# Kernel tuning notes

Measured on AMD Instinct MI355X. Metric: run time of the kernel, lower is better.

The kernel has to match this reference:

```python
import jax, jax.numpy as jnp
import numpy as np
import math

NUM_HEADS = 16
NUM_KV_HEADS = 4
HEAD_DIM = 128
HIDDEN = 2048
ROPE_BASE = 10000.0


def setup_inputs() -> dict:
    key = jax.random.key(0)
    ks = jax.random.split(key, 6)
    B, S = 1, 4096
    hidden_states = jax.random.normal(ks[0], (B, S, HIDDEN), dtype=jnp.float32)
    attention_mask = jnp.ones((B, S), dtype=jnp.int32)
    position_ids = jnp.broadcast_to(jnp.arange(S, dtype=jnp.int32)[None, :], (B, S))
    sc = 1.0 / math.sqrt(HIDDEN)
    wq = jax.random.normal(ks[1], (HIDDEN, NUM_HEADS * HEAD_DIM), dtype=jnp.float32) * sc
    wk = jax.random.normal(ks[2], (HIDDEN, NUM_KV_HEADS * HEAD_DIM), dtype=jnp.float32) * sc
    wv = jax.random.normal(ks[3], (HIDDEN, NUM_KV_HEADS * HEAD_DIM), dtype=jnp.float32) * sc
    wo = jax.random.normal(ks[4], (NUM_HEADS * HEAD_DIM, HIDDEN), dtype=jnp.float32) * sc
    return {"hidden_states": hidden_states, "attention_mask": attention_mask,
            "position_ids": position_ids, "wq": wq, "wk": wk, "wv": wv, "wo": wo}


def _rotate_half(x):
    x1, x2 = jnp.split(x, 2, axis=-1)
    return jnp.concatenate((-x2, x1), axis=-1)


def _rope_tables(seq_len, dtype):
    inv_freq = 1.0 / (ROPE_BASE ** (jnp.arange(0, HEAD_DIM, 2, dtype=jnp.float32) / HEAD_DIM))
    t = jnp.arange(seq_len, dtype=jnp.float32)
    freqs = jnp.outer(t, inv_freq)                       # [S, hd/2]
    emb = jnp.concatenate((freqs, freqs), axis=-1)       # [S, hd]
    return jnp.cos(emb).astype(dtype), jnp.sin(emb).astype(dtype)


def reference(hidden_states, attention_mask, position_ids, wq, wk, wv, wo):
    B, S, _ = hidden_states.shape
    dtype = hidden_states.dtype
    # projections -> [B, H, S, hd]
    q = (hidden_states @ wq).reshape(B, S, NUM_HEADS, HEAD_DIM).transpose(0, 2, 1, 3)
    k = (hidden_states @ wk).reshape(B, S, NUM_KV_HEADS, HEAD_DIM).transpose(0, 2, 1, 3)
    v = (hidden_states @ wv).reshape(B, S, NUM_KV_HEADS, HEAD_DIM).transpose(0, 2, 1, 3)
    # RoPE
    cos_t, sin_t = _rope_tables(S, dtype)
    cos = cos_t[position_ids][:, None]                   # [B,1,S,hd]
    sin = sin_t[position_ids][:, None]
    q = q * cos + _rotate_half(q) * sin
    k = k * cos + _rotate_half(k) * sin
    # GQA repeat
    n_rep = NUM_HEADS // NUM_KV_HEADS
    k = jnp.repeat(k, n_rep, axis=1)
    v = jnp.repeat(v, n_rep, axis=1)
    # scores + causal mask + padding mask
    scores = jnp.einsum('bhqd,bhkd->bhqk', q, k) / math.sqrt(HEAD_DIM)
    neg = jnp.finfo(scores.dtype).min
    causal = jnp.triu(jnp.full((S, S), neg, dtype=scores.dtype), k=1)
    scores = scores + causal[None, None]
    pad = (1.0 - attention_mask.astype(scores.dtype))[:, None, None, :] * neg
    scores = scores + pad
    attn = jax.nn.softmax(scores.astype(jnp.float32), axis=-1).astype(dtype)
    out = jnp.einsum('bhqk,bhkd->bhqd', attn, v)
    out = out.transpose(0, 2, 1, 3).reshape(B, S, NUM_HEADS * HEAD_DIM)
    return out @ wo
```

## Files before the change

### kernel.cpp

```cpp
#include <hip/hip_runtime.h>
#include <cstdint>
#include <cstddef>

typedef unsigned short ushort_t;
typedef short    bf16x8 __attribute__((ext_vector_type(8)));
typedef float    f32x4  __attribute__((ext_vector_type(4)));
typedef uint4    __attribute__((may_alias)) uint4_a;
typedef ushort4  __attribute__((may_alias)) ushort4_a;
typedef float4   __attribute__((may_alias)) float4_a;
typedef float2   __attribute__((may_alias)) float2_a;
typedef unsigned __attribute__((may_alias)) uint_a;

constexpr int SEQ = 4096, HID = 2048, NHEADS = 16, NKVH = 4, HDIM = 128;
constexpr int QD  = NHEADS * HDIM;
constexpr int KVD = NKVH * HDIM;
constexpr int KVL = 2 * KVD;
constexpr int NPART = 56;

static __device__ __forceinline__ float bf2f(ushort_t u) {
    return __uint_as_float(((unsigned)u) << 16);
}
static __device__ __forceinline__ ushort_t f2bf(float f) {
    unsigned x = __float_as_uint(f);
    unsigned r = x + 0x7FFFu + ((x >> 16) & 1u);
    return (ushort_t)(r >> 16);
}
static __device__ __forceinline__ unsigned pack2(float lo, float hi) {
    return (unsigned)f2bf(lo) | ((unsigned)f2bf(hi) << 16);
}
static __device__ __forceinline__ unsigned cvt_pk(float lo, float hi) {
    unsigned r;
    asm("v_cvt_pk_bf16_f32 %0, %1, %2" : "=v"(r) : "v"(lo), "v"(hi));
    return r;
}

static __device__ __forceinline__ void gld16(const ushort_t* g, ushort_t* l) {
    __builtin_amdgcn_global_load_lds(
        (const __attribute__((address_space(1))) unsigned*)g,
        (__attribute__((address_space(3))) unsigned*)l, 16, 0, 0);
}

__global__ __launch_bounds__(256) void cast_f32_bf16(
    const float* __restrict__ in, ushort_t* __restrict__ out, int n)
{
    int i = (blockIdx.x * 256 + threadIdx.x) * 8;
    if (i >= n) return;
    float4 a = *(const float4_a*)(in + i);
    float4 b = *(const float4_a*)(in + i + 4);
    uint4 o;
    o.x = pack2(a.x, a.y); o.y = pack2(a.z, a.w);
    o.z = pack2(b.x, b.y); o.w = pack2(b.z, b.w);
    *(uint4_a*)(out + i) = o;
}

__global__ __launch_bounds__(256) void transpose_cast(
    const float* __restrict__ W, ushort_t* __restrict__ WT, int K, int N)
{
    __shared__ float tl[32][36];
    const int k0 = blockIdx.x * 32, n0 = blockIdx.y * 32;
    const int t  = threadIdx.x;
    {
        int i = t >> 3, jb = (t & 7) * 4;
        *(float4_a*)&tl[i][jb] = *(const float4_a*)(W + (size_t)(k0 + i) * N + n0 + jb);
    }
    __syncthreads();
    {
        int n = t >> 3, kb = (t & 7) * 4;
        ushort4 o;
        o.x = f2bf(tl[kb + 0][n]); o.y = f2bf(tl[kb + 1][n]);
        o.z = f2bf(tl[kb + 2][n]); o.w = f2bf(tl[kb + 3][n]);
        *(ushort4_a*)(WT + (size_t)(n0 + n) * K + k0 + kb) = o;
    }
}

__global__ __launch_bounds__(256) void transpose_cast_qkv(
    const float* __restrict__ wq, const float* __restrict__ wk,
    const float* __restrict__ wv, ushort_t* __restrict__ WT)
{
    __shared__ float tl[32][36];
    const int k0 = blockIdx.x * 32, nb = blockIdx.y * 32;
    const int t  = threadIdx.x;
    const float* W; int n0, N;
    if (nb < 2048)      { W = wq; n0 = nb;        N = QD;  }
    else if (nb < 2560) { W = wk; n0 = nb - 2048; N = KVD; }
    else                { W = wv; n0 = nb - 2560; N = KVD; }
    {
        int i = t >> 3, jb = (t & 7) * 4;
        *(float4_a*)&tl[i][jb] = *(const float4_a*)(W + (size_t)(k0 + i) * N + n0 + jb);
    }
    __syncthreads();
    {
        int n = t >> 3, kb = (t & 7) * 4;
        ushort4 o;
        o.x = f2bf(tl[kb + 0][n]); o.y = f2bf(tl[kb + 1][n]);
        o.z = f2bf(tl[kb + 2][n]); o.w = f2bf(tl[kb + 3][n]);
        *(ushort4_a*)(WT + (size_t)(nb + n) * HID + k0 + kb) = o;
    }
}

__global__ __launch_bounds__(256) void gemm_mfma(
    const ushort_t* __restrict__ A, int lda,
    const ushort_t* __restrict__ Bt, int ldb,
    void* __restrict__ C1, int ld1, void* __restrict__ C2, int ld2,
    int split, int N, int K, int out_f32)
{
    __shared__ ushort_t as[128 * 32];
    __shared__ ushort_t bs[128 * 32];

    const int t    = threadIdx.x;
    const int mb   = blockIdx.y * 128, nb = blockIdx.x * 128;
    const int w    = t >> 6, lane = t & 63, quad = lane >> 4, l15 = lane & 15;
    const int wm   = (w >> 1) * 64, wn = (w & 1) * 64;

    const int dr_row = lane >> 2, dr_c = lane & 3;
    const int rA0 = w * 16 + dr_row, rA1 = 64 + w * 16 + dr_row;
    const ushort_t* a0p = A  + (size_t)(mb + rA0) * lda + (dr_c ^ (rA0 & 3)) * 8;
    const ushort_t* a1p = A  + (size_t)(mb + rA1) * lda + (dr_c ^ (rA1 & 3)) * 8;
    const ushort_t* b0p = Bt + (size_t)(nb + rA0) * ldb + (dr_c ^ (rA0 & 3)) * 8;
    const ushort_t* b1p = Bt + (size_t)(nb + rA1) * ldb + (dr_c ^ (rA1 & 3)) * 8;
    ushort_t* asb0 = &as[(w) * 512];        ushort_t* asb1 = &as[(4 + w) * 512];
    ushort_t* bsb0 = &bs[(w) * 512];        ushort_t* bsb1 = &bs[(4 + w) * 512];

    f32x4 acc[4][4];
#pragma unroll
    for (int i = 0; i < 4; i++)
#pragma unroll
        for (int j = 0; j < 4; j++) acc[i][j] = (f32x4)0.f;

    const int chunk = quad ^ (l15 & 3);

    for (int kb = 0; kb < K; kb += 32) {
        __syncthreads();
        gld16(a0p + kb, asb0);
        gld16(a1p + kb, asb1);
        gld16(b0p + kb, bsb0);
        gld16(b1p + kb, bsb1);
        __syncthreads();

        bf16x8 af[4], bf[4];
#pragma unroll
        for (int mt = 0; mt < 4; mt++)
            af[mt] = *(const bf16x8*)&as[(wm + mt * 16 + l15) * 32 + chunk * 8];
#pragma unroll
        for (int nt = 0; nt < 4; nt++)
            bf[nt] = *(const bf16x8*)&bs[(wn + nt * 16 + l15) * 32 + chunk * 8];
#pragma unroll
        for (int mt = 0; mt < 4; mt++)
#pragma unroll
            for (int nt = 0; nt < 4; nt++)
                acc[mt][nt] = __builtin_amdgcn_mfma_f32_16x16x32_bf16(
                    af[mt], bf[nt], acc[mt][nt], 0, 0, 0);
    }

#pragma unroll
    for (int mt = 0; mt < 4; mt++)
#pragma unroll
        for (int nt = 0; nt < 4; nt++) {
            int colg = nb + wn + nt * 16 + l15;
#pragma unroll
            for (int r = 0; r < 4; r++) {
                int row = mb + wm + mt * 16 + quad * 4 + r;
                float v = acc[mt][nt][r];
                if (out_f32)            ((float*)C1)[(size_t)row * ld1 + colg] = v;
                else if (colg < split)  ((ushort_t*)C1)[(size_t)row * ld1 + colg] = f2bf(v);
                else                    ((ushort_t*)C2)[(size_t)row * ld2 + colg - split] = f2bf(v);
            }
        }
}

__global__ __launch_bounds__(256) void rope_both(
    ushort_t* __restrict__ qb, ushort_t* __restrict__ kvb,
    const int* __restrict__ pos_ids)
{
    int idx  = blockIdx.x * 256 + threadIdx.x;
    int i    = idx & 63;
    int rem  = idx >> 6;
    int hs   = rem % (NHEADS + NKVH);
    int s    = rem / (NHEADS + NKVH);
    if (s >= SEQ) return;

    float pos = (float)pos_ids[s];
    float ang = pos * __expf(-(float)i * 0.14391156831212787f);
    float c, sn;
    sincosf(ang, &sn, &c);

    ushort_t* p = (hs < NHEADS)
        ? qb  + (size_t)s * QD  + hs * HDIM
        : kvb + (size_t)s * KVL + (hs - NHEADS) * HDIM;
    float x0 = bf2f(p[i]);
    float x1 = bf2f(p[i + 64]);
    p[i]      = f2bf(x0 * c - x1 * sn);
    p[i + 64] = f2bf(x1 * c + x0 * sn);
}

__global__ __launch_bounds__(512, 4) void flash_mfma(
    const ushort_t* Q, const ushort_t* __restrict__ KV,
    const int* __restrict__ amask, ushort_t* O,
    ushort_t* __restrict__ Opart, float2* __restrict__ ML)
{
    __shared__ ushort_t ks[2][64 * 128];
    __shared__ ushort_t vt[2][128 * 72];
    __shared__ float    bias[2][64];

    const int t = threadIdx.x, w = t >> 6, lane = t & 63;
    const int quad = lane >> 4, l15 = lane & 15;
    const int h = blockIdx.x, kvh = h >> 2;
    const int s = blockIdx.y;
    const int kcol = kvh * HDIM, vcol = KVD + kvh * HDIM;
    const float scale2 = 0.08838834764831845f * 1.44269504088896340f;

    int tile, ktb, kte, pid;
    bool multi;
    if (s < 8)       { tile = 15 - s;        ktb = 0; kte = 2 * tile + 2; multi = false; pid = 0; }
    else if (s < 64) {
        int cs = s - 8;
        int c;
        if (cs < 24) { tile = 16 + cs / 3; c = cs - (tile - 16) * 3; }
        else         { int d = cs - 24; tile = 24 + (d >> 2); c = d & 3; }
        int nkt = 2 * tile + 2;
        ktb = c * 16; kte = (ktb + 16 < nkt) ? ktb + 16 : nkt;
        multi = true; pid = h * NPART + cs;
    }
    else             { tile = 7 - (s - 64);  ktb = 0; kte = 2 * tile + 2; multi = false; pid = 0; }

    const int q0  = tile * 128;
    const int q0w = q0 + w * 16;

    const int kRow = w * 4 + quad;
    const int klc  = l15 ^ (kRow & 7);
    const int vkp  = t & 31,  vdg = t >> 5;

    int bpi[4];
#pragma unroll
    for (int t4 = 0; t4 < 4; t4++)
        bpi[t4] = ((2 * (quad & 1) + (t4 >> 1)) * 16 + l15) * 4;
    const bool hi_half = (quad >> 1) != 0;

    int pco[4];
#pragma unroll
    for (int c = 0; c < 4; c++)
        pco[c] = ((4 * c + quad) ^ (l15 & 7)) * 8;

    bf16x8 qf[4];
    {
        const ushort_t* qp = Q + (size_t)(q0w + l15) * QD + h * HDIM;
#pragma unroll
        for (int c = 0; c < 4; c++)
            qf[c] = *(const bf16x8*)(qp + c * 32 + quad * 8);
    }

    f32x4 accO[8];
#pragma unroll
    for (int j = 0; j < 8; j++) accO[j] = (f32x4)0.f;
    float m_s = -1e30f, l_s = 0.f;

    uint4 va, vb;
    float bst = 0.f;
    auto stage_k = [&](int kt, int b) {
        const ushort_t* g0 = KV + (size_t)(kt * 64 + kRow) * KVL + kcol + klc * 8;
        gld16(g0, &ks[b][w * 512]);
        gld16(g0 + (size_t)32 * KVL, &ks[b][4096 + w * 512]);
    };
    auto vload = [&](int kt) {
        const ushort_t* vp = KV + (size_t)(kt * 64 + 2 * vkp) * KVL + vcol + vdg * 8;
        va = *(const uint4_a*)vp;
        vb = *(const uint4_a*)(vp + KVL);
        bst = (t < 64) ? (amask[kt * 64 + t] ? 0.f : -1e30f) : 0.f;
    };
    auto vstore = [&](int b) {
        unsigned aw[4] = {va.x, va.y, va.z, va.w};
        unsigned bw[4] = {vb.x, vb.y, vb.z, vb.w};
#pragma unroll
        for (int i = 0; i < 4; i++) {
            *(uint_a*)&vt[b][(vdg * 8 + 2 * i) * 72 + 2 * vkp] =
                (aw[i] & 0xFFFFu) | (bw[i] << 16);
            *(uint_a*)&vt[b][(vdg * 8 + 2 * i + 1) * 72 + 2 * vkp] =
                (aw[i] >> 16) | (bw[i] & 0xFFFF0000u);
        }
        if (t < 64) bias[b][t] = bst;
    };

    stage_k(ktb, 0);
    vload(ktb);
    vstore(0);
    __syncthreads();

    for (int kt = ktb; kt < kte; kt++) {
        const int cur = (kt - ktb) & 1;
        const int k0 = kt * 64;
        const bool more = (kt + 1 < kte);
        if (more) {
            stage_k(kt + 1, cur ^ 1);
            vload(kt + 1);
        }

        if (k0 <= q0w + 15) {
            f32x4 sx[4];
#pragma unroll
            for (int mt = 0; mt < 4; mt++) sx[mt] = (f32x4)0.f;
            __builtin_amdgcn_s_setprio(1);
#pragma unroll
            for (int c = 0; c < 4; c++)
#pragma unroll
                for (int mt = 0; mt < 4; mt++) {
                    bf16x8 kf = *(const bf16x8*)&ks[cur][(mt * 16 + l15) * 128 + pco[c]];
                    sx[mt] = __builtin_amdgcn_mfma_f32_16x16x32_bf16(kf, qf[c], sx[mt], 0, 0, 0);
                }
            __builtin_amdgcn_s_setprio(0);

            const int qg = q0w + l15;
            const bool full = (k0 + 63 <= q0w);
            float p[4][4];
            float mx = -1e30f;
#pragma unroll
            for (int mt = 0; mt < 4; mt++) {
                float4 b4 = *(const float4_a*)&bias[cur][mt * 16 + quad * 4];
                float br[4] = {b4.x, b4.y, b4.z, b4.w};
#pragma unroll
                for (int r = 0; r < 4; r++) {
                    float v = fmaf(sx[mt][r], scale2, br[r]);
                    if (!full) {
                        int kg = k0 + mt * 16 + quad * 4 + r;
                        v = (kg > qg) ? -1e30f : v;
                    }
                    p[mt][r] = v;
                    mx = fmaxf(mx, v);
                }
            }
            mx = fmaxf(mx, __shfl_xor(mx, 16));
            mx = fmaxf(mx, __shfl_xor(mx, 32));
            const bool renorm = !__all(mx <= m_s + 8.f);
            const float mnew = renorm ? fmaxf(m_s, mx) : m_s;
            float sum = 0.f;
            unsigned wlo[4], whi[4];
#pragma unroll
            for (int mt = 0; mt < 4; mt++) {
                float p0 = exp2f(p[mt][0] - mnew);
                float p1 = exp2f(p[mt][1] - mnew);
                float p2 = exp2f(p[mt][2] - mnew);
                float p3 = exp2f(p[mt][3] - mnew);
                sum += (p0 + p1) + (p2 + p3);
                wlo[mt] = cvt_pk(p0, p1);
                whi[mt] = cvt_pk(p2, p3);
            }
            sum += __shfl_xor(sum, 16);
            sum += __shfl_xor(sum, 32);

            if (renorm) {
                float alpha = exp2f(m_s - mnew);
                l_s *= alpha;
                float a0 = __shfl(alpha, quad * 4 + 0);
                float a1 = __shfl(alpha, quad * 4 + 1);
                float a2 = __shfl(alpha, quad * 4 + 2);
                float a3 = __shfl(alpha, quad * 4 + 3);
#pragma unroll
                for (int j = 0; j < 8; j++) {
                    f32x4 a = accO[j];
                    a[0] *= a0; a[1] *= a1; a[2] *= a2; a[3] *= a3;
                    accO[j] = a;
                }
            }
            m_s = mnew;
            l_s += sum;

#pragma unroll
            for (int kc = 0; kc < 2; kc++) {
                union { unsigned u[4]; bf16x8 v; } pf;
#pragma unroll
                for (int t4 = 0; t4 < 4; t4++) {
                    unsigned slo = (t4 & 1) ? whi[2 * kc]     : wlo[2 * kc];
                    unsigned shi = (t4 & 1) ? whi[2 * kc + 1] : wlo[2 * kc + 1];
                    int ra = __builtin_amdgcn_ds_bpermute(bpi[t4], (int)slo);
                    int rb = __builtin_amdgcn_ds_bpermute(bpi[t4], (int)shi);
                    pf.u[t4] = (unsigned)(hi_half ? rb : ra);
                }
                __builtin_amdgcn_s_setprio(1);
#pragma unroll
                for (int n8 = 0; n8 < 8; n8++) {
                    bf16x8 vf = *(const bf16x8*)&vt[cur][(n8 * 16 + l15) * 72 + kc * 32 + quad * 8];
                    accO[n8] = __builtin_amdgcn_mfma_f32_16x16x32_bf16(pf.v, vf, accO[n8], 0, 0, 0);
                }
                __builtin_amdgcn_s_setprio(0);
            }
        }

        if (more) vstore(cur ^ 1);
        __syncthreads();
    }

    if (!multi) {
        float linv = 1.0f / l_s;
#pragma unroll
        for (int r = 0; r < 4; r++) {
            float lr = __shfl(linv, quad * 4 + r);
            int row = q0w + quad * 4 + r;
            ushort_t* op = O + (size_t)row * QD + h * HDIM;
#pragma unroll
            for (int n8 = 0; n8 < 8; n8++)
                op[n8 * 16 + l15] = f2bf(accO[n8][r] * lr);
        }
    } else {
        ushort_t* op = Opart + (size_t)pid * (128 * 128);
#pragma unroll
        for (int r = 0; r < 4; r++) {
            int row = w * 16 + quad * 4 + r;
#pragma unroll
            for (int n8 = 0; n8 < 8; n8++)
                op[row * 128 + n8 * 16 + l15] = f2bf(accO[n8][r]);
        }
        if (quad == 0)
            ML[pid * 128 + w * 16 + l15] = make_float2(m_s, l_s);
    }
}

__global__ __launch_bounds__(256) void combine_partials(
    const ushort_t* __restrict__ P, const float2* __restrict__ ML,
    ushort_t* __restrict__ O)
{
    __shared__ float wc[4][128];
    const int h = blockIdx.x >> 4, tt = blockIdx.x & 15, tile = 16 + tt;
    const int nc = (tile < 24) ? 3 : 4;
    const int pid0 = h * NPART + ((tile < 24) ? tt * 3 : 24 + (tile - 24) * 4);
    const int tid = threadIdx.x;

    if (tid < 128) {
        const int row = tid;
        float m_[4], l_[4];
        float M = -1e30f;
#pragma unroll
        for (int c = 0; c < 4; c++) {
            if (c < nc) {
                float2 v = *(const float2_a*)&ML[(pid0 + c) * 128 + row];
                m_[c] = v.x; l_[c] = v.y; M = fmaxf(M, v.x);
            } else { m_[c] = -1e30f; l_[c] = 0.f; }
        }
        float L = 0.f, wgt[4];
#pragma unroll
        for (int c = 0; c < 4; c++) { wgt[c] = exp2f(m_[c] - M); L += wgt[c] * l_[c]; }
        const float inv = 1.0f / L;
#pragma unroll
        for (int c = 0; c < 4; c++) wc[c][row] = (c < nc) ? wgt[c] * inv : 0.f;
    }
    __syncthreads();

#pragma unroll
    for (int p = 0; p < 4; p++) {
        const int idx = p * 256 + tid;
        const int row = idx >> 3, seg = idx & 7;
        const size_t pb = (size_t)row * 128 + seg * 16;
        float acc[16];
#pragma unroll
        for (int j = 0; j < 16; j++) acc[j] = 0.f;
#pragma unroll
        for (int c = 0; c < 4; c++) {
            if (c < nc) {
                const ushort_t* pp = P + (size_t)(pid0 + c) * (128 * 128) + pb;
                uint4 v0 = *(const uint4_a*)pp;
                uint4 v1 = *(const uint4_a*)(pp + 8);
                const float wv_ = wc[c][row];
                unsigned u[8] = {v0.x, v0.y, v0.z, v0.w, v1.x, v1.y, v1.z, v1.w};
#pragma unroll
                for (int j = 0; j < 8; j++) {
                    acc[2 * j]     += wv_ * bf2f((ushort_t)(u[j] & 0xFFFFu));
                    acc[2 * j + 1] += wv_ * bf2f((ushort_t)(u[j] >> 16));
                }
            }
        }
        ushort_t* op = O + (size_t)(tile * 128 + row) * QD + h * HDIM + seg * 16;
        uint4 o0, o1;
        o0.x = pack2(acc[0],  acc[1]);  o0.y = pack2(acc[2],  acc[3]);
        o0.z = pack2(acc[4],  acc[5]);  o0.w = pack2(acc[6],  acc[7]);
        o1.x = pack2(acc[8],  acc[9]);  o1.y = pack2(acc[10], acc[11]);
        o1.z = pack2(acc[12], acc[13]); o1.w = pack2(acc[14], acc[15]);
        *(uint4_a*)op       = o0;
        *(uint4_a*)(op + 8) = o1;
    }
}

extern "C" void kernel_launch(void* const* d_in, const int* in_sizes, int n_in,
                              void* d_out, int out_size, void* d_ws, size_t ws_size,
                              hipStream_t stream)
{
    const float* x     = (const float*)d_in[0];
    const int*   amask = (const int*)d_in[1];
    const int*   pos   = (const int*)d_in[2];
    const float* wq    = (const float*)d_in[3];
    const float* wk    = (const float*)d_in[4];
    const float* wv    = (const float*)d_in[5];
    const float* wo    = (const float*)d_in[6];
    float* out = (float*)d_out;

    ushort_t* wqkvT = (ushort_t*)d_out;
    ushort_t* xb    = wqkvT + (size_t)3072 * HID;

    ushort_t* qbuf  = (ushort_t*)d_ws;
    ushort_t* kvbuf = qbuf + (size_t)SEQ * QD;
    ushort_t* woT   = kvbuf;

    ushort_t* opart = (ushort_t*)d_out;
    float2*   mlbuf = (float2*)((char*)d_out + (size_t)16 * NPART * 128 * 128 * 2);

    cast_f32_bf16<<<SEQ * HID / 8 / 256, 256, 0, stream>>>(x, xb, SEQ * HID);
    transpose_cast_qkv<<<dim3(HID / 32, 3072 / 32), 256, 0, stream>>>(wq, wk, wv, wqkvT);

    gemm_mfma<<<dim3(3072 / 128, SEQ / 128), 256, 0, stream>>>(
        xb, HID, wqkvT, HID, qbuf, QD, kvbuf, KVL, QD, 3072, HID, 0);

    rope_both<<<SEQ * (NHEADS + NKVH) * 64 / 256, 256, 0, stream>>>(qbuf, kvbuf, pos);

    flash_mfma<<<dim3(NHEADS, 72), 512, 0, stream>>>(
        qbuf, kvbuf, amask, qbuf, opart, mlbuf);
    combine_partials<<<dim3(256), 256, 0, stream>>>(opart, mlbuf, qbuf);

    transpose_cast<<<dim3(QD / 32, HID / 32), 256, 0, stream>>>(wo, woT, QD, HID);
    gemm_mfma<<<dim3(HID / 128, SEQ / 128), 256, 0, stream>>>(
        qbuf, QD, woT, QD, out, HID, out, HID, HID, HID, QD, 1);
}
```

Baseline: 424.6 us.

## Add 256x256-tile double-buffered MFMA GEMM for QKV projection

Adds a new gemm256 kernel with 512 threads, 256x256 output tiles, a BK=64 double-buffered LDS pipeline, XOR-swizzled shared layout, and four compute phases per k-step using barriers and setprio to interleave loads with MFMA. It replaces the 128x128 gemm_mfma only for the QKV projection, which gets more data reuse per tile and fewer global loads. The grid drops to 12x16=192 blocks, which may underfill the CUs on the MI355X, and the larger LDS footprint (64 KB per block) and higher register count reduce occupancy.

```diff
diff --git a/kernel.cpp b/kernel.cpp
--- a/kernel.cpp
+++ b/kernel.cpp
@@ -161,6 +161,177 @@
             for (int r = 0; r < 4; r++) {
                 int row = mb + wm + mt * 16 + quad * 4 + r;
                 float v = acc[mt][nt][r];
+                if (out_f32)            ((float*)C1)[(size_t)row * ld1 + colg] = v;
+                else if (colg < split)  ((ushort_t*)C1)[(size_t)row * ld1 + colg] = f2bf(v);
+                else                    ((ushort_t*)C2)[(size_t)row * ld2 + colg - split] = f2bf(v);
+            }
+        }
+}
+
+__global__ __launch_bounds__(512, 2) void gemm256(
+    const ushort_t* __restrict__ A, int lda,
+    const ushort_t* __restrict__ Bt, int ldb,
+    void* __restrict__ C1, int ld1, void* __restrict__ C2, int ld2,
+    int split, int K, int out_f32)
+{
+    __shared__ ushort_t as[2][2][8192];
+    __shared__ ushort_t bs[2][2][8192];
+
+    const int t = threadIdx.x;
+    const int w = t >> 6, lane = t & 63, quad = lane >> 4, l15 = lane & 15;
+    const int wr = w >> 2, wc = w & 3;
+    const int mb = blockIdx.y * 256, nb = blockIdx.x * 256;
+
+    const int arow = t >> 3;
+    const int achk = ((t & 7) ^ (arow & 7)) * 8;
+    const ushort_t* a0 = A  + (size_t)(mb + arow) * lda + achk;
+    const ushort_t* a1 = A  + (size_t)(mb + 128 + arow) * lda + achk;
+    const ushort_t* b0 = Bt + (size_t)(nb + arow) * ldb + achk;
+    const ushort_t* b1 = Bt + (size_t)(nb + 128 + arow) * ldb + achk;
+
+    auto stageA = [&](int kt, int h, int b) {
+        const ushort_t* s = (h ? a1 : a0) + kt * 64;
+        gld16(s, &as[b][h][w * 512]);
+        gld16(s + (size_t)64 * lda, &as[b][h][4096 + w * 512]);
+    };
+    auto stageB = [&](int kt, int h, int b) {
+        const ushort_t* s = (h ? b1 : b0) + kt * 64;
+        gld16(s, &bs[b][h][w * 512]);
+        gld16(s + (size_t)64 * ldb, &bs[b][h][4096 + w * 512]);
+    };
+
+    int aoff[2], boff[2];
+#pragma unroll
+    for (int ks = 0; ks < 2; ks++) {
+        int pc = ((ks * 4 + quad) ^ (l15 & 7)) * 8;
+        aoff[ks] = l15 * 64 + pc;
+        boff[ks] = (wc & 1) * 4096 + l15 * 64 + pc;
+    }
+
+    f32x4 acc[8][4];
+#pragma unroll
+    for (int i = 0; i < 8; i++)
+#pragma unroll
+        for (int j = 0; j < 4; j++) acc[i][j] = (f32x4)0.f;
+
+    const int nkt = K >> 6;
+
+    stageA(0, 0, 0); stageB(0, 0, 0);
+    stageA(0, 1, 0); stageB(0, 1, 0);
+    asm volatile("s_waitcnt vmcnt(0)" ::: "memory");
+    __builtin_amdgcn_s_barrier();
+
+    for (int kt = 0; kt < nkt; ++kt) {
+        const int par = kt & 1;
+        const bool more = (kt + 1 < nkt);
+        const ushort_t* ab = &as[par][wr][0];
+        const ushort_t* bb = &bs[par][wc >> 1][0];
+
+        bf16x8 af[4][2], bf[2][2];
+
+        if (more) { stageA(kt + 1, 0, par ^ 1); stageB(kt + 1, 0, par ^ 1); }
+#pragma unroll
+        for (int mr = 0; mr < 4; mr++)
+#pragma unroll
+            for (int ks = 0; ks < 2; ks++)
+                af[mr][ks] = *(const bf16x8*)&ab[mr * 1024 + aoff[ks]];
+#pragma unroll
+        for (int nr = 0; nr < 2; nr++)
+#pragma unroll
+            for (int ks = 0; ks < 2; ks++)
+                bf[nr][ks] = *(const bf16x8*)&bb[nr * 1024 + boff[ks]];
+        __builtin_amdgcn_s_barrier();
+        asm volatile("s_waitcnt lgkmcnt(0)" ::: "memory");
+        __builtin_amdgcn_sched_barrier(0);
+        __builtin_amdgcn_s_setprio(1);
+#pragma unroll
+        for (int ks = 0; ks < 2; ks++)
+#pragma unroll
+            for (int mr = 0; mr < 4; mr++)
+#pragma unroll
+                for (int nr = 0; nr < 2; nr++)
+                    acc[mr][nr] = __builtin_amdgcn_mfma_f32_16x16x32_bf16(
+                        af[mr][ks], bf[nr][ks], acc[mr][nr], 0, 0, 0);
+        __builtin_amdgcn_s_setprio(0);
+        __builtin_amdgcn_s_barrier();
+
+        if (more) { stageA(kt + 1, 1, par ^ 1); stageB(kt + 1, 1, par ^ 1); }
+#pragma unroll
+        for (int nr = 0; nr < 2; nr++)
+#pragma unroll
+            for (int ks = 0; ks < 2; ks++)
+                bf[nr][ks] = *(const bf16x8*)&bb[(nr + 2) * 1024 + boff[ks]];
+        __builtin_amdgcn_s_barrier();
+        asm volatile("s_waitcnt lgkmcnt(0)" ::: "memory");
+        __builtin_amdgcn_sched_barrier(0);
+        __builtin_amdgcn_s_setprio(1);
+#pragma unroll
+        for (int ks = 0; ks < 2; ks++)
+#pragma unroll
+            for (int mr = 0; mr < 4; mr++)
+#pragma unroll
+                for (int nr = 0; nr < 2; nr++)
+                    acc[mr][nr + 2] = __builtin_amdgcn_mfma_f32_16x16x32_bf16(
+                        af[mr][ks], bf[nr][ks], acc[mr][nr + 2], 0, 0, 0);
+        __builtin_amdgcn_s_setprio(0);
+        __builtin_amdgcn_s_barrier();
+
+#pragma unroll
+        for (int mr = 0; mr < 4; mr++)
+#pragma unroll
+            for (int ks = 0; ks < 2; ks++)
+                af[mr][ks] = *(const bf16x8*)&ab[(mr + 4) * 1024 + aoff[ks]];
+#pragma unroll
+        for (int nr = 0; nr < 2; nr++)
+#pragma unroll
+            for (int ks = 0; ks < 2; ks++)
+                bf[nr][ks] = *(const bf16x8*)&bb[nr * 1024 + boff[ks]];
+        __builtin_amdgcn_s_barrier();
+        asm volatile("s_waitcnt lgkmcnt(0)" ::: "memory");
+        __builtin_amdgcn_sched_barrier(0);
+        __builtin_amdgcn_s_setprio(1);
+#pragma unroll
+        for (int ks = 0; ks < 2; ks++)
+#pragma unroll
+            for (int mr = 0; mr < 4; mr++)
+#pragma unroll
+                for (int nr = 0; nr < 2; nr++)
+                    acc[mr + 4][nr] = __builtin_amdgcn_mfma_f32_16x16x32_bf16(
+                        af[mr][ks], bf[nr][ks], acc[mr + 4][nr], 0, 0, 0);
+        __builtin_amdgcn_s_setprio(0);
+        __builtin_amdgcn_s_barrier();
+
+#pragma unroll
+        for (int nr = 0; nr < 2; nr++)
+#pragma unroll
+            for (int ks = 0; ks < 2; ks++)
+                bf[nr][ks] = *(const bf16x8*)&bb[(nr + 2) * 1024 + boff[ks]];
+        __builtin_amdgcn_s_barrier();
+        asm volatile("s_waitcnt lgkmcnt(0)" ::: "memory");
+        __builtin_amdgcn_sched_barrier(0);
+        __builtin_amdgcn_s_setprio(1);
+#pragma unroll
+        for (int ks = 0; ks < 2; ks++)
+#pragma unroll
+            for (int mr = 0; mr < 4; mr++)
+#pragma unroll
+                for (int nr = 0; nr < 2; nr++)
+                    acc[mr + 4][nr + 2] = __builtin_amdgcn_mfma_f32_16x16x32_bf16(
+                        af[mr][ks], bf[nr][ks], acc[mr + 4][nr + 2], 0, 0, 0);
+        __builtin_amdgcn_s_setprio(0);
+        if (more) asm volatile("s_waitcnt vmcnt(0)" ::: "memory");
+        __builtin_amdgcn_s_barrier();
+    }
+
+#pragma unroll
+    for (int mrep = 0; mrep < 8; mrep++)
+#pragma unroll
+        for (int nrep = 0; nrep < 4; nrep++) {
+            int colg = nb + wc * 64 + nrep * 16 + l15;
+#pragma unroll
+            for (int r = 0; r < 4; r++) {
+                int row = mb + wr * 128 + mrep * 16 + quad * 4 + r;
+                float v = acc[mrep][nrep][r];
                 if (out_f32)            ((float*)C1)[(size_t)row * ld1 + colg] = v;
                 else if (colg < split)  ((ushort_t*)C1)[(size_t)row * ld1 + colg] = f2bf(v);
                 else                    ((ushort_t*)C2)[(size_t)row * ld2 + colg - split] = f2bf(v);
@@ -503,8 +674,8 @@
     cast_f32_bf16<<<SEQ * HID / 8 / 256, 256, 0, stream>>>(x, xb, SEQ * HID);
     transpose_cast_qkv<<<dim3(HID / 32, 3072 / 32), 256, 0, stream>>>(wq, wk, wv, wqkvT);
 
-    gemm_mfma<<<dim3(3072 / 128, SEQ / 128), 256, 0, stream>>>(
-        xb, HID, wqkvT, HID, qbuf, QD, kvbuf, KVL, QD, 3072, HID, 0);
+    gemm256<<<dim3(3072 / 256, SEQ / 256), 512, 0, stream>>>(
+        xb, HID, wqkvT, HID, qbuf, QD, kvbuf, KVL, QD, HID, 0);
 
     rope_both<<<SEQ * (NHEADS + NKVH) * 64 / 256, 256, 0, stream>>>(qbuf, kvbuf, pos);
 
```

New measurement: 445.4 us. +4.9%, slower.
